# Performance work log

Measured on AMD Instinct MI355X. Metric: run time of the kernel, lower is better.

Reference implementation:

```python
import jax, jax.numpy as jnp
import numpy as np

B, N, D = 8, 2048, 256
K = 8
NP = 1024  # num_pooled = ceil(N * 0.5)
EPS = 1e-8
TEMP = 1.0


def setup_inputs() -> dict:
    key = jax.random.key(0)
    k1, k2, k3, k4 = jax.random.split(key, 4)
    tokens = jax.random.normal(k1, (B, N, D), dtype=jnp.float32)
    timestamps = jax.random.uniform(k2, (B, N), dtype=jnp.float32)
    W1 = jax.random.normal(k3, (2 * D, 128), dtype=jnp.float32) * 0.02
    b1 = jnp.zeros((128,), dtype=jnp.float32)
    W2 = jax.random.normal(k4, (128, NP), dtype=jnp.float32) * 0.02
    b2 = jnp.zeros((NP,), dtype=jnp.float32)
    return {"tokens": tokens, "timestamps": timestamps, "W1": W1, "b1": b1, "W2": W2, "b2": b2}


def _build_adjacency(tokens):
    # mutual-kNN graph on cosine similarity -> [B, N, N] float 0/1
    tn = tokens / (jnp.linalg.norm(tokens, axis=-1, keepdims=True) + EPS)
    sim = jnp.einsum("bnd,bmd->bnm", tn, tn)
    sim = jnp.where(jnp.eye(N, dtype=bool)[None], -jnp.inf, sim)  # no self (add_self=False)
    _, idx = jax.lax.top_k(sim, K)  # [B, N, K]
    bi = jnp.arange(B)[:, None, None]
    ri = jnp.arange(N)[None, :, None]
    adj = jnp.zeros((B, N, N), dtype=bool).at[bi, ri, idx].set(True)
    adj = adj & jnp.swapaxes(adj, 1, 2)  # mutual
    return adj.astype(jnp.float32)


def reference(tokens, timestamps, W1, b1, W2, b2):
    adjacency = _build_adjacency(tokens)

    # degree-normalized aggregation (use_gnn=True)
    degree = jnp.clip(adjacency.sum(axis=-1, keepdims=True), 1.0, None)
    agg = jnp.matmul(adjacency / degree, tokens)  # [B, N, D]
    features = jnp.concatenate([tokens, agg], axis=-1)  # [B, N, 2D]

    # assignment MLP (Linear -> exact GELU -> Linear), softmax over clusters
    h = jax.nn.gelu(features @ W1 + b1, approximate=False)
    logits = h @ W2 + b2  # [B, N, NP]
    assign = jax.nn.softmax(logits / TEMP, axis=-1)

    # soft-assignment pooling
    pooled_tokens = jnp.einsum("bnp,bnd->bpd", assign, tokens)  # [B, NP, D]
    pooled_t = jnp.einsum("bnp,bn->bp", assign, timestamps)  # [B, NP]

    # reorder pooled tokens by pooled timestamp
    sort_idx = jnp.argsort(pooled_t, axis=-1)
    pooled_tokens = jnp.take_along_axis(pooled_tokens, sort_idx[..., None], axis=1)
    pooled_t = jnp.take_along_axis(pooled_t, sort_idx, axis=1)

    # auxiliary losses
    assign_st = jnp.einsum("bnp,bmp->bnm", assign, assign)
    link_loss = jnp.mean((assign_st - adjacency) ** 2)
    entropy = jnp.mean(-jnp.sum(assign * jnp.log(assign + EPS), axis=-1))

    return pooled_tokens, pooled_t, link_loss, entropy
```

## Files before the change

### kernel.cpp

```cpp
#include <hip/hip_runtime.h>
#include <math.h>

#define B_ 8
#define N_ 2048
#define D_ 256
#define K_ 8
#define NP_ 1024
#define H_ 128
#define EPS_ 1e-8f
#define NEG_INF_ (-1e30f)

typedef unsigned int uint;
typedef unsigned short ushort;
typedef __attribute__((ext_vector_type(4))) float f32x4;
typedef __attribute__((ext_vector_type(8))) short short8;

__device__ __forceinline__ float gelu_exact(float x) {
    return 0.5f * x * (1.0f + erff(x * 0.70710678118654752440f));
}

__device__ __forceinline__ float dot4(float4 a, float4 b) {
    return a.x * b.x + a.y * b.y + a.z * b.z + a.w * b.w;
}

__device__ __forceinline__ ushort f2bf(float f) {
    uint u = __float_as_uint(f);
    u = (u + 0x7FFFu + ((u >> 16) & 1u)) >> 16;
    return (ushort)u;
}

__device__ __forceinline__ void gll16(const void* g, void* l) {
    __builtin_amdgcn_global_load_lds(
        (const __attribute__((address_space(1))) unsigned int*)g,
        (__attribute__((address_space(3))) unsigned int*)l, 16, 0, 0);
}

__device__ __forceinline__ float bsum256(float* red, int t, float v) {
    red[t] = v;
    __syncthreads();
#pragma unroll
    for (int s = 128; s > 0; s >>= 1) {
        if (t < s) red[t] += red[t + s];
        __syncthreads();
    }
    float r = red[0];
    __syncthreads();
    return r;
}

__device__ __forceinline__ float bmax256(float* red, int t, float v) {
    red[t] = v;
    __syncthreads();
#pragma unroll
    for (int s = 128; s > 0; s >>= 1) {
        if (t < s) red[t] = fmaxf(red[t], red[t + s]);
        __syncthreads();
    }
    float r = red[0];
    __syncthreads();
    return r;
}

__device__ __forceinline__ uint mono16(uint v) {
    return (v & 0x8000u) ? ((~v) & 0xFFFFu) : (v | 0x8000u);
}

__global__ __launch_bounds__(256) void k_norm(const float* __restrict__ tokens,
                                              float* __restrict__ tn,
                                              ushort* __restrict__ tnbf) {
    int row = blockIdx.x;
    int t = threadIdx.x;
    __shared__ float red[256];
    float x = tokens[(size_t)row * D_ + t];
    float ss = bsum256(red, t, x * x);
    float nrm = sqrtf(ss) + EPS_;
    float y = x / nrm;
    tn[(size_t)row * D_ + t] = y;
    tnbf[(size_t)row * D_ + t] = f2bf(y);
}

#define SCW_ 72
#define INSK_(L) { bool in_ = key > L; uint tm_ = L; L = in_ ? key : L; key = in_ ? tm_ : key; }
#define INS16_ INSK_(l0) INSK_(l1) INSK_(l2) INSK_(l3) INSK_(l4) INSK_(l5) INSK_(l6) INSK_(l7) \
               INSK_(l8) INSK_(l9) INSK_(l10) INSK_(l11) INSK_(l12) INSK_(l13) INSK_(l14) INSK_(l15)
#define INSM_ INSK_(m0) INSK_(m1) INSK_(m2) INSK_(m3) INSK_(m4) INSK_(m5) INSK_(m6) INSK_(m7) \
              INSK_(m8) INSK_(m9) INSK_(m10) INSK_(m11) INSK_(m12) INSK_(m13) INSK_(m14) INSK_(m15)

__global__ __launch_bounds__(256) void k_simtop(const ushort* __restrict__ tnbf,
                                                int* __restrict__ cands) {
    __shared__ __align__(16) char lds[53760];
    char* Bs = lds + 16384;
    ushort* sc = (ushort*)(lds + 49152);
    uint* mg = (uint*)(lds + 16384);

    int bid = blockIdx.x;
    int b = bid & 7;
    int panel = bid >> 3;
    int i0 = panel * 32;
    int t = threadIdx.x;
    int lane = t & 63;
    int wv = t >> 6;
    int rh = wv & 1, ch = wv >> 1;
    const char* tbb = (const char*)(tnbf + (size_t)b * N_ * D_);

#pragma unroll
    for (int c = 0; c < 4; ++c) {
        int e = (wv * 4 + c) * 64 + lane;
        int row = e >> 5, g = e & 31;
        gll16(tbb + (size_t)(i0 + row) * 512 + ((g ^ (row & 15)) << 4),
              lds + (wv * 4 + c) * 1024);
    }
    const char* gsrc[8];
#pragma unroll
    for (int c = 0; c < 8; ++c) {
        int e = (wv * 8 + c) * 64 + lane;
        int row = e >> 5, g = e & 31;
        gsrc[c] = tbb + (size_t)row * 512 + ((g ^ (row & 15)) << 4);
    }
#pragma unroll
    for (int c = 0; c < 8; ++c) {
        gll16(gsrc[c], Bs + (wv * 8 + c) * 1024);
        gsrc[c] += 32768;
    }
    asm volatile("s_waitcnt vmcnt(0)" ::: "memory");
    __syncthreads();

    int selrow = t >> 3;
    int selcs = t & 7;
    int gi = i0 + selrow;
    uint l0=0,l1=0,l2=0,l3=0,l4=0,l5=0,l6=0,l7=0,l8=0,l9=0,l10=0,l11=0,l12=0,l13=0,l14=0,l15=0;
    uint rth = 0;

    int arow = rh * 16 + (lane & 15);
    int brow0 = ch * 32 + (lane & 15);
    int brow1 = brow0 + 16;
    int scw = (rh * 16 + (lane >> 4) * 4) * SCW_ + ch * 32 + (lane & 15);

    for (int jt = 0; jt < 32; ++jt) {
        f32x4 acc0 = (f32x4){0.f, 0.f, 0.f, 0.f};
        f32x4 acc1 = (f32x4){0.f, 0.f, 0.f, 0.f};
#pragma unroll
        for (int ks = 0; ks < 8; ++ks) {
            int u = ks * 4 + (lane >> 4);
            short8 af = *(const short8*)(lds + arow * 512 + ((u ^ (arow & 15)) << 4));
            short8 bf0 = *(const short8*)(Bs + brow0 * 512 + ((u ^ (lane & 15)) << 4));
            short8 bf1 = *(const short8*)(Bs + brow1 * 512 + ((u ^ (lane & 15)) << 4));
            acc0 = __builtin_amdgcn_mfma_f32_16x16x32_bf16(af, bf0, acc0, 0, 0, 0);
            acc1 = __builtin_amdgcn_mfma_f32_16x16x32_bf16(af, bf1, acc1, 0, 0, 0);
        }
#pragma unroll
        for (int v = 0; v < 4; ++v) sc[scw + v * SCW_] = f2bf(acc0[v]);
#pragma unroll
        for (int v = 0; v < 4; ++v) sc[scw + v * SCW_ + 16] = f2bf(acc1[v]);
        __syncthreads();

        if (jt < 31) {
#pragma unroll
            for (int c = 0; c < 8; ++c) {
                gll16(gsrc[c], Bs + (wv * 8 + c) * 1024);
                gsrc[c] += 32768;
            }
        }
        int j0 = jt * 64;
        int sbase = selrow * SCW_;
        uint gate = l15 > rth ? l15 : rth;
#pragma unroll
        for (int jj = 0; jj < 8; ++jj) {
            int col = selcs + jj * 8;
            int j = j0 + col;
            uint sv = sc[sbase + col];
            if (j != gi) {
                uint key = (mono16(sv) << 16) | (65535u - (uint)j);
                if (key > gate) {
                    INS16_
                    gate = l15 > rth ? l15 : rth;
                }
            }
        }
        {
            uint m = l15;
            m = m > (uint)__shfl_xor((int)m, 1) ? m : (uint)__shfl_xor((int)m, 1);
            m = m > (uint)__shfl_xor((int)m, 2) ? m : (uint)__shfl_xor((int)m, 2);
            m = m > (uint)__shfl_xor((int)m, 4) ? m : (uint)__shfl_xor((int)m, 4);
            rth = m;
        }
        asm volatile("s_waitcnt vmcnt(0)" ::: "memory");
        __syncthreads();
    }

    uint* ml = mg + (size_t)t * 17;
    ml[0]=l0; ml[1]=l1; ml[2]=l2; ml[3]=l3; ml[4]=l4; ml[5]=l5; ml[6]=l6; ml[7]=l7;
    ml[8]=l8; ml[9]=l9; ml[10]=l10; ml[11]=l11; ml[12]=l12; ml[13]=l13; ml[14]=l14; ml[15]=l15;
    __syncthreads();
    if (selcs == 0) {
        uint m0=0,m1=0,m2=0,m3=0,m4=0,m5=0,m6=0,m7=0,m8=0,m9=0,m10=0,m11=0,m12=0,m13=0,m14=0,m15=0;
        const uint* base = mg + (size_t)(selrow * 8) * 17;
#pragma unroll
        for (int s2 = 0; s2 < 8; ++s2) {
            const uint* lp = base + s2 * 17;
            for (int q = 0; q < 16; ++q) {
                uint key = lp[q];
                if (key <= m15) break;
                INSM_
            }
        }
        int* crow = cands + ((size_t)b * N_ + gi) * 16;
        crow[0]=(int)(65535u-(m0&0xFFFFu));   crow[1]=(int)(65535u-(m1&0xFFFFu));
        crow[2]=(int)(65535u-(m2&0xFFFFu));   crow[3]=(int)(65535u-(m3&0xFFFFu));
        crow[4]=(int)(65535u-(m4&0xFFFFu));   crow[5]=(int)(65535u-(m5&0xFFFFu));
        crow[6]=(int)(65535u-(m6&0xFFFFu));   crow[7]=(int)(65535u-(m7&0xFFFFu));
        crow[8]=(int)(65535u-(m8&0xFFFFu));   crow[9]=(int)(65535u-(m9&0xFFFFu));
        crow[10]=(int)(65535u-(m10&0xFFFFu)); crow[11]=(int)(65535u-(m11&0xFFFFu));
        crow[12]=(int)(65535u-(m12&0xFFFFu)); crow[13]=(int)(65535u-(m13&0xFFFFu));
        crow[14]=(int)(65535u-(m14&0xFFFFu)); crow[15]=(int)(65535u-(m15&0xFFFFu));
    }
}

__global__ __launch_bounds__(64) void k_rescore(const float* __restrict__ tn,
                                                const int* __restrict__ cands,
                                                int* __restrict__ topk) {
    int row = blockIdx.x;
    int b = row >> 11;
    int lane = threadIdx.x;
    int j = cands[(size_t)row * 16 + (lane & 15)];
    float s = 0.f;
    if (lane < 16) {
        const float* ti = tn + (size_t)row * D_;
        const float* tj = tn + ((size_t)(b << 11) + j) * D_;
        for (int d = 0; d < D_; d += 4) {
            float4 u = *(const float4*)(tj + d);
            float4 w = *(const float4*)(ti + d);
            s += dot4(u, w);
        }
    }
    float dv[16];
    int jv[16];
#pragma unroll
    for (int c = 0; c < 16; ++c) {
        dv[c] = __shfl(s, c);
        jv[c] = __shfl(j, c);
    }
    uint used = 0;
    for (int r = 0; r < 8; ++r) {
        float bv = -1e38f;
        int bj = 1 << 30, bc = -1;
#pragma unroll
        for (int c = 0; c < 16; ++c) {
            bool av = !(used & (1u << c));
            bool better = av && (dv[c] > bv || (dv[c] == bv && jv[c] < bj));
            bv = better ? dv[c] : bv;
            bj = better ? jv[c] : bj;
            bc = better ? c : bc;
        }
        used |= 1u << bc;
        if (lane == 0) topk[(size_t)row * K_ + r] = bj;
    }
}

__global__ __launch_bounds__(64) void k_adj_agg(const float* __restrict__ tokens,
                                                const int* __restrict__ topk,
                                                int* __restrict__ nbr,
                                                int* __restrict__ deg,
                                                float* __restrict__ agg) {
    int row = blockIdx.x;
    int b = row >> 11;
    int i = row & (N_ - 1);
    int t = threadIdx.x;
    __shared__ int s_cand[K_];
    __shared__ int s_nbr[K_];
    __shared__ int s_deg;
    if (t < K_) {
        int j = topk[(size_t)row * K_ + t];
        const int* tj = topk + ((size_t)(b * N_ + j)) * K_;
        bool mut = false;
#pragma unroll
        for (int k = 0; k < K_; ++k) mut = mut || (tj[k] == i);
        s_cand[t] = mut ? j : -1;
    }
    __syncthreads();
    if (t == 0) {
        int d = 0;
#pragma unroll
        for (int k = 0; k < K_; ++k)
            if (s_cand[k] >= 0) s_nbr[d++] = s_cand[k];
        s_deg = d;
    }
    __syncthreads();
    int dgi = s_deg;
    const float* tb = tokens + (size_t)b * N_ * D_;
    float a0 = 0, a1 = 0, a2 = 0, a3 = 0;
    for (int k = 0; k < dgi; ++k) {
        float4 v = *(const float4*)(tb + (size_t)s_nbr[k] * D_ + t * 4);
        a0 += v.x; a1 += v.y; a2 += v.z; a3 += v.w;
    }
    float inv = 1.0f / (float)(dgi > 0 ? dgi : 1);
    *(float4*)(agg + (size_t)row * D_ + t * 4) = make_float4(a0 * inv, a1 * inv, a2 * inv, a3 * inv);
    if (t < K_) nbr[(size_t)row * K_ + t] = (t < dgi) ? s_nbr[t] : -1;
    if (t == 0) deg[row] = dgi;
}

__global__ __launch_bounds__(256) void k_tokT(const float* __restrict__ tokens,
                                              ushort* __restrict__ tokT) {
    int b = blockIdx.z;
    int n0 = blockIdx.x * 32, d0 = blockIdx.y * 32;
    __shared__ float tile[32][33];
    int t = threadIdx.x;
#pragma unroll
    for (int q = 0; q < 4; ++q) {
        int e = q * 256 + t;
        int r = e >> 5, c = e & 31;
        tile[r][c] = tokens[((size_t)b * N_ + n0 + r) * D_ + d0 + c];
    }
    __syncthreads();
#pragma unroll
    for (int q = 0; q < 4; ++q) {
        int e = q * 256 + t;
        int r = e >> 5, c = e & 31;
        tokT[((size_t)b * D_ + d0 + r) * N_ + n0 + c] = f2bf(tile[c][r]);
    }
}

__global__ __launch_bounds__(256) void k_asT(const float* __restrict__ assign,
                                             ushort* __restrict__ assignT) {
    int b = blockIdx.z;
    int n0 = blockIdx.x * 32, p0 = blockIdx.y * 32;
    __shared__ float tile[32][33];
    int t = threadIdx.x;
#pragma unroll
    for (int q = 0; q < 4; ++q) {
        int e = q * 256 + t;
        int r = e >> 5, c = e & 31;
        tile[r][c] = assign[((size_t)b * N_ + n0 + r) * NP_ + p0 + c];
    }
    __syncthreads();
#pragma unroll
    for (int q = 0; q < 4; ++q) {
        int e = q * 256 + t;
        int r = e >> 5, c = e & 31;
        assignT[((size_t)b * NP_ + p0 + r) * N_ + n0 + c] = f2bf(tile[c][r]);
    }
}

__global__ __launch_bounds__(256) void k_mlp1(const float* __restrict__ tokens,
                                              const float* __restrict__ agg,
                                              const float* __restrict__ W1,
                                              const float* __restrict__ b1,
                                              float* __restrict__ h) {
    int row0 = blockIdx.x * 16;
    int t = threadIdx.x;
    int col = t & 127;
    int half = t >> 7;
    __shared__ float feat[16][2 * D_];
    for (int e = t; e < 16 * 2 * D_; e += 256) {
        int r = e >> 9, c = e & 511;
        feat[r][c] = (c < D_) ? tokens[(size_t)(row0 + r) * D_ + c]
                              : agg[(size_t)(row0 + r) * D_ + (c - D_)];
    }
    __syncthreads();
    const float* fr = &feat[half * 8][0];
    float bias = b1[col];
    float a0 = bias, a1 = bias, a2 = bias, a3 = bias, a4 = bias, a5 = bias, a6 = bias, a7 = bias;
    for (int i = 0; i < 2 * D_; i += 4) {
        float w0 = W1[(size_t)(i + 0) * H_ + col];
        float w1 = W1[(size_t)(i + 1) * H_ + col];
        float w2 = W1[(size_t)(i + 2) * H_ + col];
        float w3 = W1[(size_t)(i + 3) * H_ + col];
        float4 f0 = *(const float4*)(fr + 0 * 512 + i);
        float4 f1 = *(const float4*)(fr + 1 * 512 + i);
        float4 f2 = *(const float4*)(fr + 2 * 512 + i);
        float4 f3 = *(const float4*)(fr + 3 * 512 + i);
        float4 f4 = *(const float4*)(fr + 4 * 512 + i);
        float4 f5 = *(const float4*)(fr + 5 * 512 + i);
        float4 f6 = *(const float4*)(fr + 6 * 512 + i);
        float4 f7 = *(const float4*)(fr + 7 * 512 + i);
        a0 += f0.x * w0; a0 += f0.y * w1; a0 += f0.z * w2; a0 += f0.w * w3;
        a1 += f1.x * w0; a1 += f1.y * w1; a1 += f1.z * w2; a1 += f1.w * w3;
        a2 += f2.x * w0; a2 += f2.y * w1; a2 += f2.z * w2; a2 += f2.w * w3;
        a3 += f3.x * w0; a3 += f3.y * w1; a3 += f3.z * w2; a3 += f3.w * w3;
        a4 += f4.x * w0; a4 += f4.y * w1; a4 += f4.z * w2; a4 += f4.w * w3;
        a5 += f5.x * w0; a5 += f5.y * w1; a5 += f5.z * w2; a5 += f5.w * w3;
        a6 += f6.x * w0; a6 += f6.y * w1; a6 += f6.z * w2; a6 += f6.w * w3;
        a7 += f7.x * w0; a7 += f7.y * w1; a7 += f7.z * w2; a7 += f7.w * w3;
    }
    int rb = row0 + half * 8;
    h[(size_t)(rb + 0) * H_ + col] = gelu_exact(a0);
    h[(size_t)(rb + 1) * H_ + col] = gelu_exact(a1);
    h[(size_t)(rb + 2) * H_ + col] = gelu_exact(a2);
    h[(size_t)(rb + 3) * H_ + col] = gelu_exact(a3);
    h[(size_t)(rb + 4) * H_ + col] = gelu_exact(a4);
    h[(size_t)(rb + 5) * H_ + col] = gelu_exact(a5);
    h[(size_t)(rb + 6) * H_ + col] = gelu_exact(a6);
    h[(size_t)(rb + 7) * H_ + col] = gelu_exact(a7);
}

__global__ __launch_bounds__(256) void k_mlp2f(const float* __restrict__ hmat,
                                               const float* __restrict__ W2,
                                               const float* __restrict__ b2,
                                               float* __restrict__ assign,
                                               float* __restrict__ ent_partial) {
    int row0 = blockIdx.x * 16;
    int t = threadIdx.x;
    __shared__ float hsT[128 * 20];
    __shared__ float red2[16][256];
    __shared__ float red[256];
    for (int e = t; e < 16 * H_; e += 256) {
        int r = e >> 7, i = e & 127;
        hsT[i * 20 + r] = hmat[(size_t)row0 * H_ + e];
    }
    __syncthreads();
    float acc[16][4];
#pragma unroll
    for (int s = 0; s < 4; ++s) {
        float bb = b2[s * 256 + t];
#pragma unroll
        for (int r = 0; r < 16; ++r) acc[r][s] = bb;
    }
#pragma unroll 4
    for (int i = 0; i < H_; ++i) {
        float w0 = W2[(size_t)i * NP_ + t];
        float w1 = W2[(size_t)i * NP_ + 256 + t];
        float w2 = W2[(size_t)i * NP_ + 512 + t];
        float w3 = W2[(size_t)i * NP_ + 768 + t];
        float hv[16];
        *(float4*)&hv[0] = *(const float4*)&hsT[i * 20 + 0];
        *(float4*)&hv[4] = *(const float4*)&hsT[i * 20 + 4];
        *(float4*)&hv[8] = *(const float4*)&hsT[i * 20 + 8];
        *(float4*)&hv[12] = *(const float4*)&hsT[i * 20 + 12];
#pragma unroll
        for (int r = 0; r < 16; ++r) {
            acc[r][0] += hv[r] * w0; acc[r][1] += hv[r] * w1;
            acc[r][2] += hv[r] * w2; acc[r][3] += hv[r] * w3;
        }
    }
#pragma unroll
    for (int r = 0; r < 16; ++r)
        red2[r][t] = fmaxf(fmaxf(acc[r][0], acc[r][1]), fmaxf(acc[r][2], acc[r][3]));
    __syncthreads();
#pragma unroll
    for (int s = 128; s > 0; s >>= 1) {
        if (t < s) {
#pragma unroll
            for (int r = 0; r < 16; ++r) red2[r][t] = fmaxf(red2[r][t], red2[r][t + s]);
        }
        __syncthreads();
    }
#pragma unroll
    for (int r = 0; r < 16; ++r) {
        float m = red2[r][0];
        acc[r][0] -= m; acc[r][1] -= m; acc[r][2] -= m; acc[r][3] -= m;
    }
    __syncthreads();
#pragma unroll
    for (int r = 0; r < 16; ++r)
        red2[r][t] = expf(acc[r][0]) + expf(acc[r][1]) + expf(acc[r][2]) + expf(acc[r][3]);
    __syncthreads();
#pragma unroll
    for (int s = 128; s > 0; s >>= 1) {
        if (t < s) {
#pragma unroll
            for (int r = 0; r < 16; ++r) red2[r][t] += red2[r][t + s];
        }
        __syncthreads();
    }
    float entv = 0.f;
#pragma unroll
    for (int r = 0; r < 16; ++r) {
        float tot = red2[r][0];
        float inv = 1.0f / tot;
        float p0 = expf(acc[r][0]) * inv, p1 = expf(acc[r][1]) * inv;
        float p2 = expf(acc[r][2]) * inv, p3 = expf(acc[r][3]) * inv;
        float* arow = assign + (size_t)(row0 + r) * NP_;
        arow[t] = p0; arow[256 + t] = p1; arow[512 + t] = p2; arow[768 + t] = p3;
        entv -= p0 * logf(p0 + EPS_) + p1 * logf(p1 + EPS_) + p2 * logf(p2 + EPS_) + p3 * logf(p3 + EPS_);
    }
    float bs = bsum256(red, t, entv);
    if (t == 0) ent_partial[blockIdx.x] = bs;
}

__device__ __forceinline__ void stage8k(const ushort* __restrict__ A,
                                        const ushort* __restrict__ B,
                                        int kb, char* lA, char* lB, int wv, int lane) {
#pragma unroll
    for (int c = 0; c < 2; ++c) {
        int e = (wv * 2 + c) * 64 + lane;
        int row = e >> 3, g = e & 7;
        size_t go = (size_t)row * N_ + kb + ((g ^ (row & 7)) << 3);
        gll16(A + go, lA + (wv * 2 + c) * 1024);
        gll16(B + go, lB + (wv * 2 + c) * 1024);
    }
}

__device__ __forceinline__ void gemm64g(const ushort* __restrict__ A,
                                        const ushort* __restrict__ B,
                                        f32x4 acc[2][2], char* lds) {
    int t = threadIdx.x;
    int lane = t & 63;
    int wv = t >> 6;
    int wm = wv >> 1, wn = wv & 1;
    stage8k(A, B, 0, lds, lds + 8192, wv, lane);
    for (int kb = 0; kb < N_; kb += 64) {
        int cur = (kb >> 6) & 1;
        char* lA = lds + cur * 16384;
        char* lB = lA + 8192;
        asm volatile("s_waitcnt vmcnt(0)" ::: "memory");
        __syncthreads();
        if (kb + 64 < N_) {
            char* nA = lds + (cur ^ 1) * 16384;
            stage8k(A, B, kb + 64, nA, nA + 8192, wv, lane);
        }
#pragma unroll
        for (int ks = 0; ks < 2; ++ks) {
            short8 afr[2], bfr[2];
#pragma unroll
            for (int f = 0; f < 2; ++f) {
                int rowA = wm * 32 + f * 16 + (lane & 15);
                int u = ks * 4 + (lane >> 4);
                afr[f] = *(const short8*)(lA + rowA * 128 + ((u ^ (rowA & 7)) << 4));
                int rowB = wn * 32 + f * 16 + (lane & 15);
                bfr[f] = *(const short8*)(lB + rowB * 128 + ((u ^ (rowB & 7)) << 4));
            }
#pragma unroll
            for (int fm = 0; fm < 2; ++fm)
#pragma unroll
                for (int fn = 0; fn < 2; ++fn)
                    acc[fm][fn] = __builtin_amdgcn_mfma_f32_16x16x32_bf16(
                        afr[fm], bfr[fn], acc[fm][fn], 0, 0, 0);
        }
    }
}

__global__ __launch_bounds__(256) void k_pool64(const ushort* __restrict__ assignT,
                                                const ushort* __restrict__ tokT,
                                                float* __restrict__ pooled) {
    __shared__ __align__(16) char lds[32768];
    int bid = blockIdx.x;
    int b = bid & 7;
    int tile = bid >> 3;
    int p0 = (tile >> 2) * 64, d0 = (tile & 3) * 64;
    const ushort* A = assignT + ((size_t)b * NP_ + p0) * N_;
    const ushort* Bp = tokT + ((size_t)b * D_ + d0) * N_;
    f32x4 acc[2][2];
#pragma unroll
    for (int x = 0; x < 2; ++x)
#pragma unroll
        for (int y = 0; y < 2; ++y) acc[x][y] = (f32x4){0.f, 0.f, 0.f, 0.f};
    gemm64g(A, Bp, acc, lds);
    int lane = threadIdx.x & 63;
    int wid = threadIdx.x >> 6;
    int wm = wid >> 1, wn = wid & 1;
#pragma unroll
    for (int fm = 0; fm < 2; ++fm)
#pragma unroll
        for (int fn = 0; fn < 2; ++fn) {
            int p = p0 + wm * 32 + fm * 16 + (lane >> 4) * 4;
            int d = d0 + wn * 32 + fn * 16 + (lane & 15);
#pragma unroll
            for (int v = 0; v < 4; ++v)
                pooled[((size_t)b * NP_ + p + v) * D_ + d] = acc[fm][fn][v];
        }
}

__global__ __launch_bounds__(256) void k_gram64(const ushort* __restrict__ assignT,
                                                float* __restrict__ gram_partial) {
    __shared__ __align__(16) char lds[32768];
    __shared__ float red[256];
    int bid = blockIdx.x;
    int b = bid & 7;
    int idx = bid >> 3;
    int ti = 0, rem = idx;
    while (rem >= 16 - ti) { rem -= 16 - ti; ++ti; }
    int tj = ti + rem;
    const ushort* A = assignT + ((size_t)b * NP_ + ti * 64) * N_;
    const ushort* Bp = assignT + ((size_t)b * NP_ + tj * 64) * N_;
    f32x4 acc[2][2];
#pragma unroll
    for (int x = 0; x < 2; ++x)
#pragma unroll
        for (int y = 0; y < 2; ++y) acc[x][y] = (f32x4){0.f, 0.f, 0.f, 0.f};
    gemm64g(A, Bp, acc, lds);
    float lsum = 0.f;
#pragma unroll
    for (int x = 0; x < 2; ++x)
#pragma unroll
        for (int y = 0; y < 2; ++y)
#pragma unroll
            for (int v = 0; v < 4; ++v) lsum += acc[x][y][v] * acc[x][y][v];
    float bs = bsum256(red, threadIdx.x, lsum);
    if (threadIdx.x == 0) gram_partial[(size_t)b * 136 + idx] = (ti == tj ? 1.0f : 2.0f) * bs;
}

__global__ __launch_bounds__(256) void k_poolt_part(const float* __restrict__ assign,
                                                    const float* __restrict__ ts,
                                                    float* __restrict__ part) {
    int bid = blockIdx.x;
    int b = bid & 7, ck = bid >> 3;
    int t = threadIdx.x;
    const float* A = assign + ((size_t)b * N_ + (size_t)ck * 64) * NP_;
    const float* T = ts + (size_t)b * N_ + (size_t)ck * 64;
    float4 acc = make_float4(0.f, 0.f, 0.f, 0.f);
    for (int n = 0; n < 64; ++n) {
        float4 v = *(const float4*)(A + (size_t)n * NP_ + t * 4);
        float tv = T[n];
        acc.x += v.x * tv; acc.y += v.y * tv; acc.z += v.z * tv; acc.w += v.w * tv;
    }
    *(float4*)(part + ((size_t)(b * 32 + ck)) * NP_ + t * 4) = acc;
}

__global__ __launch_bounds__(256) void k_poolt_red(const float* __restrict__ part,
                                                   float* __restrict__ pooled_t_u) {
    int b = blockIdx.x;
    int t = threadIdx.x;
    float4 acc = make_float4(0.f, 0.f, 0.f, 0.f);
    for (int ck = 0; ck < 32; ++ck) {
        float4 v = *(const float4*)(part + ((size_t)(b * 32 + ck)) * NP_ + t * 4);
        acc.x += v.x; acc.y += v.y; acc.z += v.z; acc.w += v.w;
    }
    *(float4*)(pooled_t_u + (size_t)b * NP_ + t * 4) = acc;
}

__global__ __launch_bounds__(64) void k_edge(const float* __restrict__ assign,
                                             const int* __restrict__ nbr,
                                             const int* __restrict__ deg,
                                             float* __restrict__ edge_partial) {
    int row = blockIdx.x;
    int t = threadIdx.x;
    int dgi = deg[row];
    int b = row >> 11;
    float acc = 0.f;
    if (dgi > 0) {
        const float* ai = assign + (size_t)row * NP_;
        float areg[16];
#pragma unroll
        for (int q = 0; q < 16; ++q) areg[q] = ai[q * 64 + t];
        for (int k = 0; k < dgi; ++k) {
            int j = nbr[(size_t)row * K_ + k];
            const float* aj = assign + ((size_t)(b * N_ + j)) * NP_;
#pragma unroll
            for (int q = 0; q < 16; ++q) acc += areg[q] * aj[q * 64 + t];
        }
    }
#pragma unroll
    for (int s = 32; s > 0; s >>= 1) acc += __shfl_down(acc, s);
    if (t == 0) edge_partial[row] = acc;
}

__global__ __launch_bounds__(256) void k_sort(const float* __restrict__ pooled_t_u,
                                              float* __restrict__ out_pt,
                                              int* __restrict__ sortidx) {
    int b = blockIdx.x;
    int t = threadIdx.x;
    __shared__ float val[NP_];
    __shared__ int sidx[NP_];
    for (int e = t; e < NP_; e += 256) { val[e] = pooled_t_u[(size_t)b * NP_ + e]; sidx[e] = e; }
    __syncthreads();
    for (int k = 2; k <= NP_; k <<= 1) {
        for (int j = k >> 1; j > 0; j >>= 1) {
            for (int e = t; e < NP_; e += 256) {
                int l = e ^ j;
                if (l > e) {
                    bool up = ((e & k) == 0);
                    float v1 = val[e], v2 = val[l];
                    int i1 = sidx[e], i2 = sidx[l];
                    bool sw = up ? ((v1 > v2) || (v1 == v2 && i1 > i2))
                                 : ((v1 < v2) || (v1 == v2 && i1 < i2));
                    if (sw) { val[e] = v2; val[l] = v1; sidx[e] = i2; sidx[l] = i1; }
                }
            }
            __syncthreads();
        }
    }
    for (int e = t; e < NP_; e += 256) {
        out_pt[(size_t)b * NP_ + e] = val[e];
        sortidx[(size_t)b * NP_ + e] = sidx[e];
    }
}

__global__ __launch_bounds__(64) void k_gather(const float* __restrict__ pooledU,
                                               const int* __restrict__ sortidx,
                                               float* __restrict__ out) {
    int bp = blockIdx.x;
    int b = bp >> 10;
    int src = sortidx[bp];
    const float4* s = (const float4*)(pooledU + ((size_t)(b << 10) + src) * D_);
    float4* d = (float4*)(out + (size_t)bp * D_);
    d[threadIdx.x] = s[threadIdx.x];
}

__global__ __launch_bounds__(256) void k_fin(const float* __restrict__ gram_partial,
                                             const float* __restrict__ edge_partial,
                                             const float* __restrict__ ent_partial,
                                             const int* __restrict__ deg,
                                             float* __restrict__ out2) {
    int t = threadIdx.x;
    __shared__ float red[256];
    float t1 = 0.f, t2 = 0.f, t3 = 0.f, ent = 0.f;
    for (int i = t; i < 136 * B_; i += 256) t1 += gram_partial[i];
    for (int i = t; i < B_ * N_; i += 256) t2 += edge_partial[i];
    for (int i = t; i < (B_ * N_) / 16; i += 256) ent += ent_partial[i];
    for (int i = t; i < B_ * N_; i += 256) t3 += (float)deg[i];
    t1 = bsum256(red, t, t1);
    t2 = bsum256(red, t, t2);
    t3 = bsum256(red, t, t3);
    ent = bsum256(red, t, ent);
    if (t == 0) {
        out2[0] = (t1 - 2.f * t2 + t3) / (float)((size_t)B_ * N_ * N_);
        out2[1] = ent / (float)(B_ * N_);
    }
}

extern "C" void kernel_launch(void* const* d_in, const int* in_sizes, int n_in,
                              void* d_out, int out_size, void* d_ws, size_t ws_size,
                              hipStream_t stream) {
    const float* tokens = (const float*)d_in[0];
    const float* tstamp = (const float*)d_in[1];
    const float* W1 = (const float*)d_in[2];
    const float* b1 = (const float*)d_in[3];
    const float* W2 = (const float*)d_in[4];
    const float* b2 = (const float*)d_in[5];
    float* out = (float*)d_out;

    char* wsp = (char*)d_ws;
    size_t off = 0;
    auto alloc = [&](size_t bytes) -> void* {
        void* p = wsp + off;
        off += (bytes + 255) & ~(size_t)255;
        return p;
    };
    float* tn = (float*)alloc(sizeof(float) * (size_t)B_ * N_ * D_);
    float* agg = tn;
    float* assign = (float*)alloc(sizeof(float) * (size_t)B_ * N_ * NP_);
    ushort* tnbf = (ushort*)alloc(sizeof(ushort) * (size_t)B_ * N_ * D_);
    ushort* tokT = tnbf;
    float* hbuf = (float*)alloc(sizeof(float) * (size_t)B_ * N_ * H_);
    ushort* assignT = (ushort*)alloc(sizeof(ushort) * (size_t)B_ * NP_ * N_);
    float* pooledU = (float*)alloc(sizeof(float) * (size_t)B_ * NP_ * D_);
    float* pooltU = (float*)alloc(sizeof(float) * (size_t)B_ * NP_);
    float* poolt_part = (float*)alloc(sizeof(float) * (size_t)B_ * 32 * NP_);
    int* candbuf = (int*)alloc(sizeof(int) * (size_t)B_ * N_ * 16);
    int* topkbuf = (int*)alloc(sizeof(int) * (size_t)B_ * N_ * K_);
    int* nbrbuf = (int*)alloc(sizeof(int) * (size_t)B_ * N_ * K_);
    int* degbuf = (int*)alloc(sizeof(int) * (size_t)B_ * N_);
    int* sortidx = (int*)alloc(sizeof(int) * (size_t)B_ * NP_);
    float* gram_p = (float*)alloc(sizeof(float) * 136 * B_);
    float* edge_p = (float*)alloc(sizeof(float) * (size_t)B_ * N_);
    float* ent_p = (float*)alloc(sizeof(float) * (size_t)(B_ * N_) / 16);

    k_norm<<<B_ * N_, 256, 0, stream>>>(tokens, tn, tnbf);
    k_simtop<<<512, 256, 0, stream>>>(tnbf, candbuf);
    k_rescore<<<B_ * N_, 64, 0, stream>>>(tn, candbuf, topkbuf);
    k_adj_agg<<<B_ * N_, 64, 0, stream>>>(tokens, topkbuf, nbrbuf, degbuf, agg);
    k_tokT<<<dim3(N_ / 32, D_ / 32, B_), 256, 0, stream>>>(tokens, tokT);
    k_mlp1<<<(B_ * N_) / 16, 256, 0, stream>>>(tokens, agg, W1, b1, hbuf);
    k_mlp2f<<<(B_ * N_) / 16, 256, 0, stream>>>(hbuf, W2, b2, assign, ent_p);
    k_asT<<<dim3(N_ / 32, NP_ / 32, B_), 256, 0, stream>>>(assign, assignT);
    k_pool64<<<512, 256, 0, stream>>>(assignT, tokT, pooledU);
    k_poolt_part<<<256, 256, 0, stream>>>(assign, tstamp, poolt_part);
    k_poolt_red<<<B_, 256, 0, stream>>>(poolt_part, pooltU);
    k_gram64<<<1088, 256, 0, stream>>>(assignT, gram_p);
    k_edge<<<B_ * N_, 64, 0, stream>>>(assign, nbrbuf, degbuf, edge_p);
    k_sort<<<B_, 256, 0, stream>>>(pooltU, out + (size_t)B_ * NP_ * D_, sortidx);
    k_gather<<<B_ * NP_, 64, 0, stream>>>(pooledU, sortidx, out);
    k_fin<<<1, 256, 0, stream>>>(gram_p, edge_p, ent_p, degbuf,
                                 out + (size_t)B_ * NP_ * D_ + (size_t)B_ * NP_);
}
```

Before: 588.1 us.

## Fuse MLP layers into one kernel and fold pooled-time reduction into sort

Merges the first MLP layer (with GELU) and the second layer plus softmax/entropy into a single kernel. The hidden activations now pass through shared memory, which is reused between the feature tile and the transposed hidden/reduction buffers, instead of making a round trip through global memory. The pooled-timestamp partial reduction is also folded into the sort kernel, removing one launch and the intermediate buffer. The cost is a larger shared-memory footprint per block, which may lower occupancy, and both GEMM phases now run in the same block.

```diff
diff --git a/kernel.cpp b/kernel.cpp
--- a/kernel.cpp
+++ b/kernel.cpp
@@ -341,23 +341,31 @@
     }
 }
 
-__global__ __launch_bounds__(256) void k_mlp1(const float* __restrict__ tokens,
-                                              const float* __restrict__ agg,
-                                              const float* __restrict__ W1,
-                                              const float* __restrict__ b1,
-                                              float* __restrict__ h) {
+__global__ __launch_bounds__(256) void k_mlp12(const float* __restrict__ tokens,
+                                               const float* __restrict__ agg,
+                                               const float* __restrict__ W1,
+                                               const float* __restrict__ b1,
+                                               const float* __restrict__ W2,
+                                               const float* __restrict__ b2,
+                                               float* __restrict__ assign,
+                                               float* __restrict__ ent_partial) {
     int row0 = blockIdx.x * 16;
     int t = threadIdx.x;
     int col = t & 127;
     int half = t >> 7;
-    __shared__ float feat[16][2 * D_];
+    __shared__ __align__(16) char smem[32768];
+    __shared__ float red[256];
+    float* feat = (float*)smem;
+    float* hsT = (float*)smem;
+    float* red2 = (float*)(smem + 10240);
+
     for (int e = t; e < 16 * 2 * D_; e += 256) {
         int r = e >> 9, c = e & 511;
-        feat[r][c] = (c < D_) ? tokens[(size_t)(row0 + r) * D_ + c]
-                              : agg[(size_t)(row0 + r) * D_ + (c - D_)];
-    }
-    __syncthreads();
-    const float* fr = &feat[half * 8][0];
+        feat[r * 512 + c] = (c < D_) ? tokens[(size_t)(row0 + r) * D_ + c]
+                                     : agg[(size_t)(row0 + r) * D_ + (c - D_)];
+    }
+    __syncthreads();
+    const float* fr = feat + (half * 8) * 512;
     float bias = b1[col];
     float a0 = bias, a1 = bias, a2 = bias, a3 = bias, a4 = bias, a5 = bias, a6 = bias, a7 = bias;
     for (int i = 0; i < 2 * D_; i += 4) {
@@ -382,32 +390,17 @@
         a6 += f6.x * w0; a6 += f6.y * w1; a6 += f6.z * w2; a6 += f6.w * w3;
         a7 += f7.x * w0; a7 += f7.y * w1; a7 += f7.z * w2; a7 += f7.w * w3;
     }
-    int rb = row0 + half * 8;
-    h[(size_t)(rb + 0) * H_ + col] = gelu_exact(a0);
-    h[(size_t)(rb + 1) * H_ + col] = gelu_exact(a1);
-    h[(size_t)(rb + 2) * H_ + col] = gelu_exact(a2);
-    h[(size_t)(rb + 3) * H_ + col] = gelu_exact(a3);
-    h[(size_t)(rb + 4) * H_ + col] = gelu_exact(a4);
-    h[(size_t)(rb + 5) * H_ + col] = gelu_exact(a5);
-    h[(size_t)(rb + 6) * H_ + col] = gelu_exact(a6);
-    h[(size_t)(rb + 7) * H_ + col] = gelu_exact(a7);
-}
-
-__global__ __launch_bounds__(256) void k_mlp2f(const float* __restrict__ hmat,
-                                               const float* __restrict__ W2,
-                                               const float* __restrict__ b2,
-                                               float* __restrict__ assign,
-                                               float* __restrict__ ent_partial) {
-    int row0 = blockIdx.x * 16;
-    int t = threadIdx.x;
-    __shared__ float hsT[128 * 20];
-    __shared__ float red2[16][256];
-    __shared__ float red[256];
-    for (int e = t; e < 16 * H_; e += 256) {
-        int r = e >> 7, i = e & 127;
-        hsT[i * 20 + r] = hmat[(size_t)row0 * H_ + e];
-    }
-    __syncthreads();
+    float g0 = gelu_exact(a0), g1 = gelu_exact(a1), g2 = gelu_exact(a2), g3 = gelu_exact(a3);
+    float g4 = gelu_exact(a4), g5 = gelu_exact(a5), g6 = gelu_exact(a6), g7 = gelu_exact(a7);
+    __syncthreads();
+    {
+        int rb = half * 8;
+        float* hp = hsT + col * 20 + rb;
+        hp[0] = g0; hp[1] = g1; hp[2] = g2; hp[3] = g3;
+        hp[4] = g4; hp[5] = g5; hp[6] = g6; hp[7] = g7;
+    }
+    __syncthreads();
+
     float acc[16][4];
 #pragma unroll
     for (int s = 0; s < 4; ++s) {
@@ -434,38 +427,39 @@
     }
 #pragma unroll
     for (int r = 0; r < 16; ++r)
-        red2[r][t] = fmaxf(fmaxf(acc[r][0], acc[r][1]), fmaxf(acc[r][2], acc[r][3]));
+        red2[r * 256 + t] = fmaxf(fmaxf(acc[r][0], acc[r][1]), fmaxf(acc[r][2], acc[r][3]));
     __syncthreads();
 #pragma unroll
     for (int s = 128; s > 0; s >>= 1) {
         if (t < s) {
 #pragma unroll
-            for (int r = 0; r < 16; ++r) red2[r][t] = fmaxf(red2[r][t], red2[r][t + s]);
+            for (int r = 0; r < 16; ++r)
+                red2[r * 256 + t] = fmaxf(red2[r * 256 + t], red2[r * 256 + t + s]);
         }
         __syncthreads();
     }
 #pragma unroll
     for (int r = 0; r < 16; ++r) {
-        float m = red2[r][0];
+        float m = red2[r * 256];
         acc[r][0] -= m; acc[r][1] -= m; acc[r][2] -= m; acc[r][3] -= m;
     }
     __syncthreads();
 #pragma unroll
     for (int r = 0; r < 16; ++r)
-        red2[r][t] = expf(acc[r][0]) + expf(acc[r][1]) + expf(acc[r][2]) + expf(acc[r][3]);
+        red2[r * 256 + t] = expf(acc[r][0]) + expf(acc[r][1]) + expf(acc[r][2]) + expf(acc[r][3]);
     __syncthreads();
 #pragma unroll
     for (int s = 128; s > 0; s >>= 1) {
         if (t < s) {
 #pragma unroll
-            for (int r = 0; r < 16; ++r) red2[r][t] += red2[r][t + s];
+            for (int r = 0; r < 16; ++r) red2[r * 256 + t] += red2[r * 256 + t + s];
         }
         __syncthreads();
     }
     float entv = 0.f;
 #pragma unroll
     for (int r = 0; r < 16; ++r) {
-        float tot = red2[r][0];
+        float tot = red2[r * 256];
         float inv = 1.0f / tot;
         float p0 = expf(acc[r][0]) * inv, p1 = expf(acc[r][1]) * inv;
         float p2 = expf(acc[r][2]) * inv, p3 = expf(acc[r][3]) * inv;
@@ -606,18 +600,6 @@
     *(float4*)(part + ((size_t)(b * 32 + ck)) * NP_ + t * 4) = acc;
 }
 
-__global__ __launch_bounds__(256) void k_poolt_red(const float* __restrict__ part,
-                                                   float* __restrict__ pooled_t_u) {
-    int b = blockIdx.x;
-    int t = threadIdx.x;
-    float4 acc = make_float4(0.f, 0.f, 0.f, 0.f);
-    for (int ck = 0; ck < 32; ++ck) {
-        float4 v = *(const float4*)(part + ((size_t)(b * 32 + ck)) * NP_ + t * 4);
-        acc.x += v.x; acc.y += v.y; acc.z += v.z; acc.w += v.w;
-    }
-    *(float4*)(pooled_t_u + (size_t)b * NP_ + t * 4) = acc;
-}
-
 __global__ __launch_bounds__(64) void k_edge(const float* __restrict__ assign,
                                              const int* __restrict__ nbr,
                                              const int* __restrict__ deg,
@@ -644,14 +626,24 @@
     if (t == 0) edge_partial[row] = acc;
 }
 
-__global__ __launch_bounds__(256) void k_sort(const float* __restrict__ pooled_t_u,
+__global__ __launch_bounds__(256) void k_sort(const float* __restrict__ part,
                                               float* __restrict__ out_pt,
                                               int* __restrict__ sortidx) {
     int b = blockIdx.x;
     int t = threadIdx.x;
     __shared__ float val[NP_];
     __shared__ int sidx[NP_];
-    for (int e = t; e < NP_; e += 256) { val[e] = pooled_t_u[(size_t)b * NP_ + e]; sidx[e] = e; }
+    {
+        float4 acc = make_float4(0.f, 0.f, 0.f, 0.f);
+        for (int ck = 0; ck < 32; ++ck) {
+            float4 v = *(const float4*)(part + ((size_t)(b * 32 + ck)) * NP_ + t * 4);
+            acc.x += v.x; acc.y += v.y; acc.z += v.z; acc.w += v.w;
+        }
+        val[t * 4 + 0] = acc.x; val[t * 4 + 1] = acc.y;
+        val[t * 4 + 2] = acc.z; val[t * 4 + 3] = acc.w;
+        sidx[t * 4 + 0] = t * 4 + 0; sidx[t * 4 + 1] = t * 4 + 1;
+        sidx[t * 4 + 2] = t * 4 + 2; sidx[t * 4 + 3] = t * 4 + 3;
+    }
     __syncthreads();
     for (int k = 2; k <= NP_; k <<= 1) {
         for (int j = k >> 1; j > 0; j >>= 1) {
@@ -731,10 +723,8 @@
     float* assign = (float*)alloc(sizeof(float) * (size_t)B_ * N_ * NP_);
     ushort* tnbf = (ushort*)alloc(sizeof(ushort) * (size_t)B_ * N_ * D_);
     ushort* tokT = tnbf;
-    float* hbuf = (float*)alloc(sizeof(float) * (size_t)B_ * N_ * H_);
     ushort* assignT = (ushort*)alloc(sizeof(ushort) * (size_t)B_ * NP_ * N_);
     float* pooledU = (float*)alloc(sizeof(float) * (size_t)B_ * NP_ * D_);
-    float* pooltU = (float*)alloc(sizeof(float) * (size_t)B_ * NP_);
     float* poolt_part = (float*)alloc(sizeof(float) * (size_t)B_ * 32 * NP_);
     int* candbuf = (int*)alloc(sizeof(int) * (size_t)B_ * N_ * 16);
     int* topkbuf = (int*)alloc(sizeof(int) * (size_t)B_ * N_ * K_);
@@ -750,15 +740,13 @@
     k_rescore<<<B_ * N_, 64, 0, stream>>>(tn, candbuf, topkbuf);
     k_adj_agg<<<B_ * N_, 64, 0, stream>>>(tokens, topkbuf, nbrbuf, degbuf, agg);
     k_tokT<<<dim3(N_ / 32, D_ / 32, B_), 256, 0, stream>>>(tokens, tokT);
-    k_mlp1<<<(B_ * N_) / 16, 256, 0, stream>>>(tokens, agg, W1, b1, hbuf);
-    k_mlp2f<<<(B_ * N_) / 16, 256, 0, stream>>>(hbuf, W2, b2, assign, ent_p);
+    k_mlp12<<<(B_ * N_) / 16, 256, 0, stream>>>(tokens, agg, W1, b1, W2, b2, assign, ent_p);
     k_asT<<<dim3(N_ / 32, NP_ / 32, B_), 256, 0, stream>>>(assign, assignT);
     k_pool64<<<512, 256, 0, stream>>>(assignT, tokT, pooledU);
     k_poolt_part<<<256, 256, 0, stream>>>(assign, tstamp, poolt_part);
-    k_poolt_red<<<B_, 256, 0, stream>>>(poolt_part, pooltU);
     k_gram64<<<1088, 256, 0, stream>>>(assignT, gram_p);
     k_edge<<<B_ * N_, 64, 0, stream>>>(assign, nbrbuf, degbuf, edge_p);
-    k_sort<<<B_, 256, 0, stream>>>(pooltU, out + (size_t)B_ * NP_ * D_, sortidx);
+    k_sort<<<B_, 256, 0, stream>>>(poolt_part, out + (size_t)B_ * NP_ * D_, sortidx);
     k_gather<<<B_ * NP_, 64, 0, stream>>>(pooledU, sortidx, out);
     k_fin<<<1, 256, 0, stream>>>(gram_p, edge_p, ent_p, degbuf,
                                  out + (size_t)B_ * NP_ * D_ + (size_t)B_ * NP_);
```

Result: no change. 581.8 us, median of 2 (-1.1%).
